# Kernel tuning notes

Hardware: AMD Instinct MI355X
Metric: run time of the kernel (lower is better)

## Reference

```python
import jax, jax.numpy as jnp
import numpy as np

B, D, H, K = 2048, 1024, 64, 3
SKIP = 4  # first 4 dims only accumulate into ai, produce no heads


def setup_inputs() -> dict:
    key = jax.random.key(0)
    ks = jax.random.split(key, 6)
    return {
        "x": jax.random.normal(ks[0], (B, D), jnp.float32),
        "W": jax.random.normal(ks[1], (H, D), jnp.float32) * (2.0 / (H + 1)) ** 0.5,
        "c": jax.random.normal(ks[2], (1, H), jnp.float32) * 0.0,
        "Vmean": jax.random.normal(ks[3], (D, H, K), jnp.float32) * (2.0 / (H + K)) ** 0.5,
        "Valpha": jax.random.normal(ks[4], (D, H, K), jnp.float32) * (2.0 / (H + K)) ** 0.5,
        "Vstd": jax.random.normal(ks[5], (D, H, K), jnp.float32) * (2.0 / (H + K)) ** 0.5,
        "bmean": jnp.zeros((D, K), jnp.float32),
        "balpha": jnp.zeros((D, K), jnp.float32),
        "bstd": jnp.zeros((D, K), jnp.float32),
    }


def reference(x, W, c, Vmean, Valpha, Vstd, bmean, balpha, bstd):
    # ai before processing dim d is c + sum_{j<d} x[:, j] * W[:, j]^T.
    # This is a cumulative sum of per-dim rank-1 contributions -> one cumsum.
    contrib = x[:, :, None] * W.T[None, :, :]          # [B, D, H]
    prefix = c[None, :, :] + jnp.cumsum(contrib, axis=1)  # prefix[:, d] = c + sum_{j<=d}
    # h_i for dim d (d >= SKIP) uses ai = prefix[:, d-1]
    h = jax.nn.relu(prefix[:, SKIP - 1:-1, :])          # [B, D-SKIP, H]

    mean = jnp.einsum("bdh,dhk->bdk", h, Vmean[SKIP:]) + bmean[SKIP:]
    std = jax.nn.sigmoid(
        jnp.einsum("bdh,dhk->bdk", h, Vstd[SKIP:]) + bstd[SKIP:]
    ) * 2.0 + 0.6  # 10**-1 + 0.5
    alpha = jax.nn.softmax(
        jnp.einsum("bdh,dhk->bdk", h, Valpha[SKIP:]) + balpha[SKIP:], axis=-1
    )
    return (mean, std, alpha)  # each [B, D-4, K]
```

## Files before the change

kernel.cpp:

```cpp
#include <hip/hip_runtime.h>
#include <hip/hip_bf16.h>

#define B 2048
#define D 1024
#define H 64
#define DOUT (D - 4)
#define T 64
#define DC 16

typedef __attribute__((ext_vector_type(8))) short short8;
typedef __attribute__((ext_vector_type(4))) float f32x4;

#define WS_S  0
#define WS_VB (T * B * H / 2)
#define WS_WT (WS_VB + D * 2 * 64 * 4)

__device__ __forceinline__ unsigned short f2h_u(float f) {
    union { _Float16 h; unsigned short u; } v; v.h = (_Float16)f; return v.u;
}
__device__ __forceinline__ float h2f_u(unsigned short s) {
    union { unsigned short u; _Float16 h; } v; v.u = s; return (float)v.h;
}
__device__ __forceinline__ unsigned short f2bf(float f) {
    union { float f; unsigned int u; } v; v.f = f;
    unsigned int r = (v.u + 0x7FFFu + ((v.u >> 16) & 1u)) >> 16;
    return (unsigned short)r;
}
__device__ __forceinline__ unsigned cvtpk_bf16(float lo, float hi) {
    unsigned d;
    asm("v_cvt_pk_bf16_f32 %0, %1, %2" : "=v"(d) : "v"(lo), "v"(hi));
    return d;
}

union U8 { unsigned u[4]; short8 s; };
union U8Q { uint4 q; short8 s; };

__global__ __launch_bounds__(256) void k_prep(const float* __restrict__ Vm,
                                              const float* __restrict__ Va,
                                              const float* __restrict__ Vs,
                                              const float* __restrict__ W,
                                              uint4* __restrict__ VbP,
                                              unsigned short* __restrict__ Wth) {
    __shared__ float vl[4][3][192];
    __shared__ float tile[64][65];
    const int tid = threadIdx.x;
    const int bid = blockIdx.x;
    if (bid < 256) {
        const int d0 = bid * 4;
#pragma unroll
        for (int q = 0; q < 9; ++q) {
            const int j = q * 256 + tid;
            if (j < 2304) {
                const int dl  = j / 576;
                const int rem = j % 576;
                const int arr = rem / 192;
                const int off = rem % 192;
                const float* src = (arr == 0) ? Vm : (arr == 1) ? Vs : Va;
                vl[dl][arr][off] = src[(size_t)(d0 + dl) * 192 + off];
            }
        }
        __syncthreads();
#pragma unroll
        for (int q = 0; q < 2; ++q) {
            const int j  = q * 256 + tid;
            const int dl = j >> 7;
            const int ks = (j >> 6) & 1;
            const int l  = j & 63;
            const int m  = l & 15;
            const int h0 = ks * 32 + (l >> 4) * 8;
            int arr = -1, k = 0;
            if (m < 3)                 { arr = 0; k = m; }
            else if (m >= 4 && m < 7)  { arr = 1; k = m - 4; }
            else if (m >= 8 && m < 11) { arr = 2; k = m - 8; }
            unsigned u[4] = {0u, 0u, 0u, 0u};
            if (arr >= 0) {
#pragma unroll
                for (int i = 0; i < 4; ++i) {
                    unsigned short lo = f2bf(vl[dl][arr][(h0 + 2 * i) * 3 + k]);
                    unsigned short hi = f2bf(vl[dl][arr][(h0 + 2 * i + 1) * 3 + k]);
                    u[i] = ((unsigned)hi << 16) | lo;
                }
            }
            VbP[((size_t)(d0 + dl) * 2 + ks) * 64 + l] = make_uint4(u[0], u[1], u[2], u[3]);
        }
    } else {
        const int d0 = (bid - 256) * 64;
        const int tx = tid & 63;
        const int ty = tid >> 6;
#pragma unroll
        for (int r = 0; r < 64; r += 4)
            tile[r + ty][tx] = W[(size_t)(r + ty) * D + d0 + tx];
        __syncthreads();
#pragma unroll
        for (int r = 0; r < 64; r += 4)
            Wth[(size_t)(d0 + r + ty) * H + tx] = f2h_u(tile[tx][r + ty]);
    }
}

__global__ __launch_bounds__(256) void k_prefix(const float* __restrict__ x,
                                                const unsigned short* __restrict__ Wth,
                                                const float* __restrict__ cvec,
                                                unsigned short* __restrict__ S) {
    const int lane = threadIdx.x & 63;
    const int w    = threadIdx.x >> 6;
    const int b    = blockIdx.x * 4 + w;

    float run = cvec[lane];
    const float* xr = x + (size_t)b * D;
    float xv = xr[lane];
    for (int c = 0; c < 16; ++c) {
        const float xnext = (c < 15) ? xr[(c + 1) * 64 + lane] : 0.f;
#pragma unroll
        for (int j = 0; j < 64; ++j) {
            const int d = c * 64 + j;
            if ((d & 15) == 4)
                S[((size_t)(d >> 4) * B + b) * H + lane] = f2h_u(run);
            const float wv = h2f_u(Wth[(size_t)d * H + lane]);
            run = fmaf(__shfl(xv, j), wv, run);
        }
        xv = xnext;
    }
}

__global__ __launch_bounds__(256, 2) void k_main(const float* __restrict__ x,
                                                 const unsigned short* __restrict__ Wth,
                                                 const unsigned short* __restrict__ S,
                                                 const uint4* __restrict__ VbP,
                                                 const float* __restrict__ bm,
                                                 const float* __restrict__ ba,
                                                 const float* __restrict__ bs,
                                                 float* __restrict__ out) {
    __shared__ float wshf[DC][64];
    __shared__ float xsf[DC][128];
    __shared__ float bshf[DC][16];

    const int tid    = threadIdx.x;
    const int lane   = tid & 63;
    const int w      = tid >> 6;
    const int t      = blockIdx.y;
    const int bx     = blockIdx.x;
    const int dstart = 16 * t + 4;
    const int dvalid = D - dstart;
    const int r      = lane & 15;
    const int qq     = lane >> 4;

    {
        {
            const unsigned* wsrc = (const unsigned*)(Wth + (size_t)dstart * H);
#pragma unroll
            for (int q = 0; q < 2; ++q) {
                const int idx = q * 256 + tid;
                if (idx < dvalid * 32) {
                    const unsigned u = wsrc[idx];
                    const int dl = idx >> 5, h = (idx & 31) * 2;
                    wshf[dl][h]     = h2f_u((unsigned short)(u & 0xffff));
                    wshf[dl][h + 1] = h2f_u((unsigned short)(u >> 16));
                }
            }
        }
        {
#pragma unroll
            for (int q = 0; q < 2; ++q) {
                const int j = q * 256 + tid;
                const int row = j >> 2, part = j & 3;
                if (part * 4 < dvalid) {
                    float4 v = *(const float4*)(x + (size_t)(bx * 128 + row) * D + dstart + part * 4);
                    xsf[part * 4 + 0][row] = v.x;
                    xsf[part * 4 + 1][row] = v.y;
                    xsf[part * 4 + 2][row] = v.z;
                    xsf[part * 4 + 3][row] = v.w;
                }
            }
        }
        {
            const int dl = tid >> 4, m = tid & 15;
            const int d = dstart + dl;
            float v = 0.f;
            if (d < D) {
                if (m < 3)                 v = bm[(size_t)d * 3 + m];
                else if (m >= 4 && m < 7)  v = bs[(size_t)d * 3 + m - 4];
                else if (m >= 8 && m < 11) v = ba[(size_t)d * 3 + m - 8];
            }
            bshf[dl][m] = v;
        }
    }

    float a_[2][2][8];
#pragma unroll
    for (int bt = 0; bt < 2; ++bt) {
#pragma unroll
        for (int ks = 0; ks < 2; ++ks) {
            const unsigned short* sp =
                S + ((size_t)t * B + bx * 128 + w * 32 + bt * 16 + r) * H + ks * 32 + qq * 8;
            uint4 u = *(const uint4*)sp;
            a_[bt][ks][0] = h2f_u((unsigned short)(u.x & 0xffff));
            a_[bt][ks][1] = h2f_u((unsigned short)(u.x >> 16));
            a_[bt][ks][2] = h2f_u((unsigned short)(u.y & 0xffff));
            a_[bt][ks][3] = h2f_u((unsigned short)(u.y >> 16));
            a_[bt][ks][4] = h2f_u((unsigned short)(u.z & 0xffff));
            a_[bt][ks][5] = h2f_u((unsigned short)(u.z >> 16));
            a_[bt][ks][6] = h2f_u((unsigned short)(u.w & 0xffff));
            a_[bt][ks][7] = h2f_u((unsigned short)(u.w >> 16));
        }
    }
    __syncthreads();

    const int nq = (t == T - 1) ? 3 : 4;
    for (int qd = 0; qd < nq; ++qd) {
        float buf[2][12];
#pragma unroll
        for (int d4 = 0; d4 < 4; ++d4) {
            const int dl = qd * 4 + d4;
            const int d  = dstart + dl;

            U8Q A0, A1;
            A0.q = VbP[((size_t)d * 2 + 0) * 64 + lane];
            A1.q = VbP[((size_t)d * 2 + 1) * 64 + lane];

            U8 bf[2][2];
#pragma unroll
            for (int bt = 0; bt < 2; ++bt)
#pragma unroll
                for (int ks = 0; ks < 2; ++ks)
#pragma unroll
                    for (int i = 0; i < 4; ++i)
                        bf[bt][ks].u[i] = cvtpk_bf16(fmaxf(a_[bt][ks][2 * i], 0.f),
                                                     fmaxf(a_[bt][ks][2 * i + 1], 0.f));

            f32x4 bias4 = ((const f32x4*)&bshf[dl][0])[qq];

            f32x4 acc[2];
#pragma unroll
            for (int bt = 0; bt < 2; ++bt) {
                acc[bt] = __builtin_amdgcn_mfma_f32_16x16x32_bf16(A0.s, bf[bt][0].s, bias4, 0, 0, 0);
                acc[bt] = __builtin_amdgcn_mfma_f32_16x16x32_bf16(A1.s, bf[bt][1].s, acc[bt], 0, 0, 0);
            }

#pragma unroll
            for (int bt = 0; bt < 2; ++bt) {
                float z0 = acc[bt][0], z1 = acc[bt][1], z2 = acc[bt][2];
                float o0 = z0, o1 = z1, o2 = z2;
                if (qq == 1) {
                    o0 = 2.f * __builtin_amdgcn_rcpf(1.f + __expf(-z0)) + 0.6f;
                    o1 = 2.f * __builtin_amdgcn_rcpf(1.f + __expf(-z1)) + 0.6f;
                    o2 = 2.f * __builtin_amdgcn_rcpf(1.f + __expf(-z2)) + 0.6f;
                } else if (qq == 2) {
                    float mx = fmaxf(z0, fmaxf(z1, z2));
                    float e0 = __expf(z0 - mx);
                    float e1 = __expf(z1 - mx);
                    float e2 = __expf(z2 - mx);
                    float inv = __builtin_amdgcn_rcpf(e0 + e1 + e2);
                    o0 = e0 * inv; o1 = e1 * inv; o2 = e2 * inv;
                }
                buf[bt][d4 * 3 + 0] = o0;
                buf[bt][d4 * 3 + 1] = o1;
                buf[bt][d4 * 3 + 2] = o2;
            }

            float4 w0a = *(const float4*)&wshf[dl][qq * 8];
            float4 w0b = *(const float4*)&wshf[dl][qq * 8 + 4];
            float4 w1a = *(const float4*)&wshf[dl][32 + qq * 8];
            float4 w1b = *(const float4*)&wshf[dl][32 + qq * 8 + 4];
#pragma unroll
            for (int bt = 0; bt < 2; ++bt) {
                const float xv = xsf[dl][w * 32 + bt * 16 + r];
                a_[bt][0][0] = fmaf(xv, w0a.x, a_[bt][0][0]);
                a_[bt][0][1] = fmaf(xv, w0a.y, a_[bt][0][1]);
                a_[bt][0][2] = fmaf(xv, w0a.z, a_[bt][0][2]);
                a_[bt][0][3] = fmaf(xv, w0a.w, a_[bt][0][3]);
                a_[bt][0][4] = fmaf(xv, w0b.x, a_[bt][0][4]);
                a_[bt][0][5] = fmaf(xv, w0b.y, a_[bt][0][5]);
                a_[bt][0][6] = fmaf(xv, w0b.z, a_[bt][0][6]);
                a_[bt][0][7] = fmaf(xv, w0b.w, a_[bt][0][7]);
                a_[bt][1][0] = fmaf(xv, w1a.x, a_[bt][1][0]);
                a_[bt][1][1] = fmaf(xv, w1a.y, a_[bt][1][1]);
                a_[bt][1][2] = fmaf(xv, w1a.z, a_[bt][1][2]);
                a_[bt][1][3] = fmaf(xv, w1a.w, a_[bt][1][3]);
                a_[bt][1][4] = fmaf(xv, w1b.x, a_[bt][1][4]);
                a_[bt][1][5] = fmaf(xv, w1b.y, a_[bt][1][5]);
                a_[bt][1][6] = fmaf(xv, w1b.z, a_[bt][1][6]);
                a_[bt][1][7] = fmaf(xv, w1b.w, a_[bt][1][7]);
            }
        }

        if (qq < 3) {
            float* ob = out + (size_t)qq * ((size_t)B * DOUT * 3);
            const size_t ioff = (size_t)(16 * t + 4 * qd) * 3;
#pragma unroll
            for (int bt = 0; bt < 2; ++bt) {
                float* p = ob + (size_t)(bx * 128 + w * 32 + bt * 16 + r) * (DOUT * 3) + ioff;
                *(float4*)(p + 0) = make_float4(buf[bt][0], buf[bt][1], buf[bt][2], buf[bt][3]);
                *(float4*)(p + 4) = make_float4(buf[bt][4], buf[bt][5], buf[bt][6], buf[bt][7]);
                *(float4*)(p + 8) = make_float4(buf[bt][8], buf[bt][9], buf[bt][10], buf[bt][11]);
            }
        }
    }
}

extern "C" void kernel_launch(void* const* d_in, const int* in_sizes, int n_in,
                              void* d_out, int out_size, void* d_ws, size_t ws_size,
                              hipStream_t stream) {
    const float* x  = (const float*)d_in[0];
    const float* W  = (const float*)d_in[1];
    const float* c  = (const float*)d_in[2];
    const float* Vm = (const float*)d_in[3];
    const float* Va = (const float*)d_in[4];
    const float* Vs = (const float*)d_in[5];
    const float* bm = (const float*)d_in[6];
    const float* ba = (const float*)d_in[7];
    const float* bs = (const float*)d_in[8];
    float* out = (float*)d_out;

    float* wsf = (float*)d_ws;
    unsigned short* S = (unsigned short*)(wsf + WS_S);
    uint4* VbP = (uint4*)(wsf + WS_VB);
    unsigned short* Wth = (unsigned short*)(wsf + WS_WT);

    k_prep<<<dim3(256 + 16), dim3(256), 0, stream>>>(Vm, Va, Vs, W, VbP, Wth);
    k_prefix<<<dim3(B / 4), dim3(256), 0, stream>>>(x, Wth, c, S);
    k_main<<<dim3(B / 128, T), dim3(256), 0, stream>>>(x, Wth, S, VbP, bm, ba, bs, out);
}
```

Baseline: 193.7 us.

## Halve d-chunk size, stage W and V weights in LDS for prefix and main

The dimension chunk per main block drops from 16 to 8, doubling the grid's T dimension and the number of prefix checkpoints stored in S. The prefix kernel now reads fp32 W directly, staging 64-dim tiles of W and x in shared memory for 8 rows per 512-thread block, and uses float4 LDS reads instead of per-element shuffles and global loads. The main kernel preloads its slice of packed V weights into LDS instead of issuing per-step global loads. The aim is shorter sequential accumulation per main block and better reuse of W. In exchange the S buffer doubles in size and more blocks are launched.

Measured after the change: 162.2 us. -16.3%, faster.

```diff
diff --git a/kernel.cpp b/kernel.cpp
--- a/kernel.cpp
+++ b/kernel.cpp
@@ -5,8 +5,8 @@
 #define D 1024
 #define H 64
 #define DOUT (D - 4)
-#define T 64
-#define DC 16
+#define T 128
+#define DC 8
 
 typedef __attribute__((ext_vector_type(8))) short short8;
 typedef __attribute__((ext_vector_type(4))) float f32x4;
@@ -33,7 +33,6 @@
 }
 
 union U8 { unsigned u[4]; short8 s; };
-union U8Q { uint4 q; short8 s; };
 
 __global__ __launch_bounds__(256) void k_prep(const float* __restrict__ Vm,
                                               const float* __restrict__ Va,
@@ -97,28 +96,44 @@
     }
 }
 
-__global__ __launch_bounds__(256) void k_prefix(const float* __restrict__ x,
-                                                const unsigned short* __restrict__ Wth,
+__global__ __launch_bounds__(512) void k_prefix(const float* __restrict__ x,
+                                                const float* __restrict__ W,
                                                 const float* __restrict__ cvec,
                                                 unsigned short* __restrict__ S) {
-    const int lane = threadIdx.x & 63;
-    const int w    = threadIdx.x >> 6;
-    const int b    = blockIdx.x * 4 + w;
+    __shared__ float wt[64 * 68];
+    __shared__ float xl[8 * 64];
+    const int tid  = threadIdx.x;
+    const int lane = tid & 63;
+    const int w    = tid >> 6;
+    const int b    = blockIdx.x * 8 + w;
 
     float run = cvec[lane];
-    const float* xr = x + (size_t)b * D;
-    float xv = xr[lane];
     for (int c = 0; c < 16; ++c) {
-        const float xnext = (c < 15) ? xr[(c + 1) * 64 + lane] : 0.f;
-#pragma unroll
-        for (int j = 0; j < 64; ++j) {
-            const int d = c * 64 + j;
-            if ((d & 15) == 4)
-                S[((size_t)(d >> 4) * B + b) * H + lane] = f2h_u(run);
-            const float wv = h2f_u(Wth[(size_t)d * H + lane]);
-            run = fmaf(__shfl(xv, j), wv, run);
-        }
-        xv = xnext;
+        __syncthreads();
+        {
+            const int h = tid >> 3, dc = (tid & 7) * 8;
+            const float* src = W + (size_t)h * D + c * 64 + dc;
+            float4 v0 = *(const float4*)src;
+            float4 v1 = *(const float4*)(src + 4);
+            float* dst = wt + h * 68 + dc;
+            *(float4*)dst = v0;
+            *(float4*)(dst + 4) = v1;
+        }
+        xl[w * 64 + lane] = x[(size_t)b * D + c * 64 + lane];
+        __syncthreads();
+#pragma unroll
+        for (int dg = 0; dg < 16; ++dg) {
+            if (dg & 1) {
+                const int t = 8 * c + (dg >> 1);
+                S[((size_t)t * B + b) * H + lane] = f2h_u(run);
+            }
+            float4 w4 = *(const float4*)(wt + lane * 68 + dg * 4);
+            float4 x4 = *(const float4*)(xl + w * 64 + dg * 4);
+            run = fmaf(x4.x, w4.x, run);
+            run = fmaf(x4.y, w4.y, run);
+            run = fmaf(x4.z, w4.z, run);
+            run = fmaf(x4.w, w4.w, run);
+        }
     }
 }
 
@@ -130,58 +145,62 @@
                                                  const float* __restrict__ ba,
                                                  const float* __restrict__ bs,
                                                  float* __restrict__ out) {
-    __shared__ float wshf[DC][64];
-    __shared__ float xsf[DC][128];
-    __shared__ float bshf[DC][16];
+    __shared__ short8 vbsh[DC][2][64];
+    __shared__ float  wshf[DC][64];
+    __shared__ float  xsf[DC][128];
+    __shared__ float  bshf[DC][16];
 
     const int tid    = threadIdx.x;
     const int lane   = tid & 63;
     const int w      = tid >> 6;
     const int t      = blockIdx.y;
     const int bx     = blockIdx.x;
-    const int dstart = 16 * t + 4;
+    const int dstart = 8 * t + 4;
     const int dvalid = D - dstart;
     const int r      = lane & 15;
     const int qq     = lane >> 4;
 
     {
         {
+            const uint4* vsrc = VbP + (size_t)dstart * 128;
+            uint4* vdst = (uint4*)vbsh;
+#pragma unroll
+            for (int q = 0; q < 4; ++q) {
+                const int j = q * 256 + tid;
+                if (j < dvalid * 128) vdst[j] = vsrc[j];
+            }
+        }
+        {
             const unsigned* wsrc = (const unsigned*)(Wth + (size_t)dstart * H);
-#pragma unroll
-            for (int q = 0; q < 2; ++q) {
-                const int idx = q * 256 + tid;
-                if (idx < dvalid * 32) {
-                    const unsigned u = wsrc[idx];
-                    const int dl = idx >> 5, h = (idx & 31) * 2;
-                    wshf[dl][h]     = h2f_u((unsigned short)(u & 0xffff));
-                    wshf[dl][h + 1] = h2f_u((unsigned short)(u >> 16));
+            if (tid < dvalid * 32) {
+                const unsigned u = wsrc[tid];
+                const int dl = tid >> 5, h = (tid & 31) * 2;
+                wshf[dl][h]     = h2f_u((unsigned short)(u & 0xffff));
+                wshf[dl][h + 1] = h2f_u((unsigned short)(u >> 16));
+            }
+        }
+        {
+            const int row = tid >> 1, part = tid & 1;
+            if (part * 4 < dvalid) {
+                float4 v = *(const float4*)(x + (size_t)(bx * 128 + row) * D + dstart + part * 4);
+                xsf[part * 4 + 0][row] = v.x;
+                xsf[part * 4 + 1][row] = v.y;
+                xsf[part * 4 + 2][row] = v.z;
+                xsf[part * 4 + 3][row] = v.w;
+            }
+        }
+        {
+            if (tid < DC * 16) {
+                const int dl = tid >> 4, m = tid & 15;
+                const int d = dstart + dl;
+                float v = 0.f;
+                if (d < D) {
+                    if (m < 3)                 v = bm[(size_t)d * 3 + m];
+                    else if (m >= 4 && m < 7)  v = bs[(size_t)d * 3 + m - 4];
+                    else if (m >= 8 && m < 11) v = ba[(size_t)d * 3 + m - 8];
                 }
-            }
-        }
-        {
-#pragma unroll
-            for (int q = 0; q < 2; ++q) {
-                const int j = q * 256 + tid;
-                const int row = j >> 2, part = j & 3;
-                if (part * 4 < dvalid) {
-                    float4 v = *(const float4*)(x + (size_t)(bx * 128 + row) * D + dstart + part * 4);
-                    xsf[part * 4 + 0][row] = v.x;
-                    xsf[part * 4 + 1][row] = v.y;
-                    xsf[part * 4 + 2][row] = v.z;
-                    xsf[part * 4 + 3][row] = v.w;
-                }
-            }
-        }
-        {
-            const int dl = tid >> 4, m = tid & 15;
-            const int d = dstart + dl;
-            float v = 0.f;
-            if (d < D) {
-                if (m < 3)                 v = bm[(size_t)d * 3 + m];
-                else if (m >= 4 && m < 7)  v = bs[(size_t)d * 3 + m - 4];
-                else if (m >= 8 && m < 11) v = ba[(size_t)d * 3 + m - 8];
-            }
-            bshf[dl][m] = v;
+                bshf[dl][m] = v;
+            }
         }
     }
 
@@ -205,17 +224,15 @@
     }
     __syncthreads();
 
-    const int nq = (t == T - 1) ? 3 : 4;
+    const int nq = (t == T - 1) ? 1 : 2;
     for (int qd = 0; qd < nq; ++qd) {
         float buf[2][12];
 #pragma unroll
         for (int d4 = 0; d4 < 4; ++d4) {
             const int dl = qd * 4 + d4;
-            const int d  = dstart + dl;
-
-            U8Q A0, A1;
-            A0.q = VbP[((size_t)d * 2 + 0) * 64 + lane];
-            A1.q = VbP[((size_t)d * 2 + 1) * 64 + lane];
+
+            short8 A0 = vbsh[dl][0][lane];
+            short8 A1 = vbsh[dl][1][lane];
 
             U8 bf[2][2];
 #pragma unroll
@@ -232,8 +249,8 @@
             f32x4 acc[2];
 #pragma unroll
             for (int bt = 0; bt < 2; ++bt) {
-                acc[bt] = __builtin_amdgcn_mfma_f32_16x16x32_bf16(A0.s, bf[bt][0].s, bias4, 0, 0, 0);
-                acc[bt] = __builtin_amdgcn_mfma_f32_16x16x32_bf16(A1.s, bf[bt][1].s, acc[bt], 0, 0, 0);
+                acc[bt] = __builtin_amdgcn_mfma_f32_16x16x32_bf16(A0, bf[bt][0].s, bias4, 0, 0, 0);
+                acc[bt] = __builtin_amdgcn_mfma_f32_16x16x32_bf16(A1, bf[bt][1].s, acc[bt], 0, 0, 0);
             }
 
 #pragma unroll
@@ -285,7 +302,7 @@
 
         if (qq < 3) {
             float* ob = out + (size_t)qq * ((size_t)B * DOUT * 3);
-            const size_t ioff = (size_t)(16 * t + 4 * qd) * 3;
+            const size_t ioff = (size_t)(8 * t + 4 * qd) * 3;
 #pragma unroll
             for (int bt = 0; bt < 2; ++bt) {
                 float* p = ob + (size_t)(bx * 128 + w * 32 + bt * 16 + r) * (DOUT * 3) + ioff;
@@ -317,6 +334,6 @@
     unsigned short* Wth = (unsigned short*)(wsf + WS_WT);
 
     k_prep<<<dim3(256 + 16), dim3(256), 0, stream>>>(Vm, Va, Vs, W, VbP, Wth);
-    k_prefix<<<dim3(B / 4), dim3(256), 0, stream>>>(x, Wth, c, S);
+    k_prefix<<<dim3(B / 8), dim3(512), 0, stream>>>(x, W, c, S);
     k_main<<<dim3(B / 128, T), dim3(256), 0, stream>>>(x, Wth, S, VbP, bm, ba, bs, out);
 }
```
